# Performance work log

Hardware: AMD Instinct MI355X
Metric: run time of the kernel (lower is better)

## Reference

```python
import jax, jax.numpy as jnp
import numpy as np

HIDDEN = 1280
NUM_HEADS = 16
HEAD_DIM = HIDDEN // NUM_HEADS  # 80
ROPE_DIM = HEAD_DIM // 2        # 40
THETA = 10000.0
SEQ = 3072


def setup_inputs() -> dict:
    key = jax.random.key(0)
    ks = jax.random.split(key, 6)
    hidden_states = jax.random.normal(ks[0], (SEQ, HIDDEN), dtype=jnp.float32)
    position_ids = jax.random.randint(ks[1], (SEQ, 2), 0, 64, dtype=jnp.int32)
    qkv_w = jax.random.normal(ks[2], (HIDDEN, 3 * HIDDEN), dtype=jnp.float32) * (HIDDEN ** -0.5)
    qkv_b = jax.random.normal(ks[3], (3 * HIDDEN,), dtype=jnp.float32) * 0.02
    o_w = jax.random.normal(ks[4], (HIDDEN, HIDDEN), dtype=jnp.float32) * (HIDDEN ** -0.5)
    o_b = jax.random.normal(ks[5], (HIDDEN,), dtype=jnp.float32) * 0.02
    return {"hidden_states": hidden_states, "position_ids": position_ids,
            "qkv_w": qkv_w, "qkv_b": qkv_b, "o_w": o_w, "o_b": o_b}


def _rotate_half(x):
    x1, x2 = jnp.split(x, 2, axis=-1)
    return jnp.concatenate([-x2, x1], axis=-1)


def reference(hidden_states, position_ids, qkv_w, qkv_b, o_w, o_b):
    seq_len = hidden_states.shape[0]
    # fused QKV projection
    qkv = hidden_states @ qkv_w + qkv_b                     # (S, 3*H*D)
    qkv = qkv.reshape(seq_len, 3, NUM_HEADS, HEAD_DIM)
    q, k, v = qkv[:, 0], qkv[:, 1], qkv[:, 2]               # each (S, h, d)
    # 2D RoPE: inv_freq over rope dim = head_dim // 2
    inv_freq = 1.0 / (THETA ** (jnp.arange(0, ROPE_DIM, 2, dtype=jnp.float32) / ROPE_DIM))
    pos = position_ids.astype(jnp.float32)
    h_freqs = jnp.outer(pos[:, 0], inv_freq)                # (S, rope/2)
    w_freqs = jnp.outer(pos[:, 1], inv_freq)                # (S, rope/2)
    freqs = jnp.concatenate([h_freqs, w_freqs], axis=-1)    # (S, rope)
    emb = jnp.concatenate([freqs, freqs], axis=-1)          # (S, head_dim)
    cos = jnp.cos(emb)[:, None, :]                          # (S, 1, d)
    sin = jnp.sin(emb)[:, None, :]
    q = q * cos + _rotate_half(q) * sin
    k = k * cos + _rotate_half(k) * sin
    # manual attention
    scaling = HEAD_DIM ** -0.5
    attn = jnp.einsum('qhd,khd->hqk', q * scaling, k)       # (h, S, S)
    attn = jax.nn.softmax(attn, axis=-1)
    out = jnp.einsum('hqk,khd->qhd', attn, v)               # (S, h, d)
    out = out.reshape(seq_len, HIDDEN)
    return out @ o_w + o_b
```

## Files before the change

### kernel.cpp

```cpp
#include <hip/hip_runtime.h>

#define SEQ  3072
#define HID  1280
#define NH   16
#define HD   80
#define NQKV 3840

typedef unsigned short u16;
typedef unsigned int u32;
typedef __attribute__((ext_vector_type(8))) short short8;
typedef __attribute__((ext_vector_type(4))) float floatx4;

__device__ __forceinline__ u16 f2bf(float x) {
    u32 u = __float_as_uint(x);
    u += 0x7fffu + ((u >> 16) & 1u);
    return (u16)(u >> 16);
}
__device__ __forceinline__ u32 packrne(float a, float b) {
    return (u32)f2bf(a) | ((u32)f2bf(b) << 16);
}

typedef const __attribute__((address_space(1))) unsigned int* gp1_t;
typedef __attribute__((address_space(3))) unsigned int* lp3_t;
__device__ __forceinline__ void gld16(const void* g, void* l) {
    __builtin_amdgcn_global_load_lds((gp1_t)g, (lp3_t)l, 16, 0, 0);
}

__device__ __forceinline__ int swz_qk(int c, int r) {
    return (c < 8) ? (c ^ (r & 7)) : (8 + ((c - 8) ^ ((r >> 1) & 3)));
}

__global__ void rope_tables_k(const int* __restrict__ pos, float* __restrict__ cosb,
                              float* __restrict__ sinb) {
    int s = blockIdx.x;
    int j = threadIdx.x;
    if (j >= 40) return;
    float p = (float)((j < 20) ? pos[s * 2] : pos[s * 2 + 1]);
    int i = (j < 20) ? j : j - 20;
    float inv = powf(10000.0f, -(float)i / 20.0f);
    float a = p * inv;
    cosb[s * 40 + j] = cosf(a);
    sinb[s * 40 + j] = sinf(a);
}

__global__ void cast_bf16_k(const float* __restrict__ x, u16* __restrict__ hi, int n) {
    int i = blockIdx.x * 256 + threadIdx.x;
    if (i >= n) return;
    hi[i] = f2bf(x[i]);
}

__global__ void transpose_cast_k(const float* __restrict__ w, u16* __restrict__ thi,
                                 int K, int N) {
    __shared__ float tile[32][33];
    int n0 = blockIdx.x * 32, k0 = blockIdx.y * 32;
    int c = threadIdx.x & 31, r8 = threadIdx.x >> 5;
    for (int rr = r8; rr < 32; rr += 8)
        tile[rr][c] = w[(size_t)(k0 + rr) * N + n0 + c];
    __syncthreads();
    for (int rr = r8; rr < 32; rr += 8)
        thi[(size_t)(n0 + rr) * K + k0 + c] = f2bf(tile[c][rr]);
}

__global__ __launch_bounds__(256, 3) void gemm_bf16_k(
    const u16* __restrict__ A, const u16* __restrict__ B,
    const float* __restrict__ bias, float* __restrict__ C,
    int M, int N, int K) {
    __shared__ u16 lA[128 * 64], lB[128 * 64];
    const int t = threadIdx.x, lane = t & 63, w = t >> 6;
    const int qi = lane & 15, quad = lane >> 4;
    const int m0 = blockIdx.y * 128, n0 = blockIdx.x * 128;
    const int wm = (w >> 1) * 64, wn = (w & 1) * 64;

    floatx4 acc[4][4];
    for (int mi = 0; mi < 4; mi++)
        for (int ni = 0; ni < 4; ni++) acc[mi][ni] = (floatx4){0.f, 0.f, 0.f, 0.f};

    const int rg = lane >> 3;
    const int ce = ((lane & 7) ^ rg) * 8;
    size_t gA[4], gB[4];
    for (int g = 0; g < 4; g++) {
        int row = w * 32 + g * 8 + rg;
        gA[g] = (size_t)(m0 + row) * K + ce;
        gB[g] = (size_t)(n0 + row) * K + ce;
    }

    for (int k0 = 0; k0 < K; k0 += 64) {
        for (int g = 0; g < 4; g++) {
            gld16(A + gA[g] + k0, &lA[(w * 32 + g * 8) * 64]);
            gld16(B + gB[g] + k0, &lB[(w * 32 + g * 8) * 64]);
        }
        __syncthreads();
        short8 af[4][2], bf[4][2];
        for (int mi = 0; mi < 4; mi++) {
            int row = wm + mi * 16 + qi;
            for (int kh = 0; kh < 2; kh++)
                af[mi][kh] = *(const short8*)&lA[row * 64 + (((kh * 4 + quad) ^ (row & 7)) << 3)];
        }
        for (int ni = 0; ni < 4; ni++) {
            int row = wn + ni * 16 + qi;
            for (int kh = 0; kh < 2; kh++)
                bf[ni][kh] = *(const short8*)&lB[row * 64 + (((kh * 4 + quad) ^ (row & 7)) << 3)];
        }
        for (int mi = 0; mi < 4; mi++)
            for (int ni = 0; ni < 4; ni++) {
                acc[mi][ni] = __builtin_amdgcn_mfma_f32_16x16x32_bf16(af[mi][0], bf[ni][0], acc[mi][ni], 0, 0, 0);
                acc[mi][ni] = __builtin_amdgcn_mfma_f32_16x16x32_bf16(af[mi][1], bf[ni][1], acc[mi][ni], 0, 0, 0);
            }
        __syncthreads();
    }
    for (int mi = 0; mi < 4; mi++)
        for (int ni = 0; ni < 4; ni++) {
            int col = n0 + wn + ni * 16 + qi;
            int rowb = m0 + wm + mi * 16 + quad * 4;
            float b = bias[col];
            for (int r = 0; r < 4; r++)
                C[(size_t)(rowb + r) * N + col] = acc[mi][ni][r] + b;
        }
}

__global__ void pack_qkv_k(const float* __restrict__ qkv, const float* __restrict__ cosb,
                           const float* __restrict__ sinb,
                           u16* __restrict__ Qs, u16* __restrict__ Ks, u16* __restrict__ Vs) {
    __shared__ float lv[80 * 65];
    const int t = threadIdx.x;
    const int h = blockIdx.y, s0 = blockIdx.x * 64;
    const float qsc = 0.11180339887498949f * 1.4426950408889634f;

    for (int i = t; i < 64 * 10; i += 256) {
        int rl = i / 10, jg = i % 10;
        int s = s0 + rl, j = jg * 4;
        const float4 cc = *(const float4*)&cosb[s * 40 + j];
        const float4 ss = *(const float4*)&sinb[s * 40 + j];
        const float* qb = qkv + (size_t)s * NQKV + h * HD;
        const float4 q1 = *(const float4*)&qb[j];
        const float4 q2 = *(const float4*)&qb[j + 40];
        const float* kb = qb + HID;
        const float4 k1 = *(const float4*)&kb[j];
        const float4 k2 = *(const float4*)&kb[j + 40];
        uint2 qo1, qo2, ko1, ko2;
        qo1.x = packrne((q1.x * cc.x - q2.x * ss.x) * qsc, (q1.y * cc.y - q2.y * ss.y) * qsc);
        qo1.y = packrne((q1.z * cc.z - q2.z * ss.z) * qsc, (q1.w * cc.w - q2.w * ss.w) * qsc);
        qo2.x = packrne((q2.x * cc.x + q1.x * ss.x) * qsc, (q2.y * cc.y + q1.y * ss.y) * qsc);
        qo2.y = packrne((q2.z * cc.z + q1.z * ss.z) * qsc, (q2.w * cc.w + q1.w * ss.w) * qsc);
        ko1.x = packrne(k1.x * cc.x - k2.x * ss.x, k1.y * cc.y - k2.y * ss.y);
        ko1.y = packrne(k1.z * cc.z - k2.z * ss.z, k1.w * cc.w - k2.w * ss.w);
        ko2.x = packrne(k2.x * cc.x + k1.x * ss.x, k2.y * cc.y + k1.y * ss.y);
        ko2.y = packrne(k2.z * cc.z + k1.z * ss.z, k2.w * cc.w + k1.w * ss.w);
        size_t base = (size_t)(h * SEQ + s) * 96;
        int c0 = j >> 3, sub0 = j & 7;
        int c1 = (j + 40) >> 3, sub1 = (j + 40) & 7;
        int p0 = swz_qk(c0, s);
        int p1 = swz_qk(c1, s);
        *(uint2*)&Qs[base + p0 * 8 + sub0] = qo1;
        *(uint2*)&Qs[base + p1 * 8 + sub1] = qo2;
        *(uint2*)&Ks[base + p0 * 8 + sub0] = ko1;
        *(uint2*)&Ks[base + p1 * 8 + sub1] = ko2;
    }
    for (int i = t; i < 64 * 2; i += 256) {
        int rl = i >> 1, cz = 10 + (i & 1);
        int s = s0 + rl;
        int pz = swz_qk(cz, s);
        size_t base = (size_t)(h * SEQ + s) * 96;
        *(uint4*)&Qs[base + pz * 8] = (uint4){0, 0, 0, 0};
        *(uint4*)&Ks[base + pz * 8] = (uint4){0, 0, 0, 0};
    }
    for (int i = t; i < 64 * 80; i += 256) {
        int rl = i / 80, d = i % 80;
        lv[d * 65 + rl] = qkv[(size_t)(s0 + rl) * NQKV + 2 * HID + h * HD + d];
    }
    __syncthreads();
    for (int i = t; i < 80 * 16; i += 256) {
        int d = i / 16, g = i % 16;
        int c2l = g * 4;
        float v0 = lv[d * 65 + c2l], v1 = lv[d * 65 + c2l + 1];
        float v2 = lv[d * 65 + c2l + 2], v3 = lv[d * 65 + c2l + 3];
        int pc = (g >> 1) ^ (d & 7);
        uint2 o;
        o.x = packrne(v0, v1);
        o.y = packrne(v2, v3);
        *(uint2*)&Vs[((size_t)h * HD + d) * SEQ + s0 + pc * 8 + (g & 1) * 4] = o;
    }
}

__global__ __launch_bounds__(256, 3) void attn_k(
    const u16* __restrict__ Qs, const u16* __restrict__ Ks, const u16* __restrict__ Vs,
    float* __restrict__ Op, float* __restrict__ lp) {
    __shared__ u16 kbuf[2][6144];
    __shared__ u16 vbuf[2][5120];
    __shared__ u16 pls[4][1024];

    const int t = threadIdx.x, lane = t & 63, w = t >> 6;
    const int qi = lane & 15, quad = lane >> 4;
    const int h = blockIdx.y, q0 = blockIdx.x * 128, ksp = blockIdx.z;
    const int kc0 = ksp * (SEQ / 2);
    u16* const kflat = &kbuf[0][0];

    {
        const u16* Qt = Qs + (size_t)(h * SEQ + q0) * 96;
        for (int j = 0; j < 6; j++) {
            int o = (w * 6 + j) * 512;
            gld16(Qt + o + lane * 8, kflat + o);
        }
    }
    __syncthreads();
    short8 bq[2][3];
    for (int qg = 0; qg < 2; qg++) {
        int row = w * 32 + qg * 16 + qi;
        for (int k3 = 0; k3 < 3; k3++) {
            int p = (k3 < 2) ? ((4 * k3 + quad) ^ (qi & 7)) : (8 + (quad ^ ((qi >> 1) & 3)));
            bq[qg][k3] = *(const short8*)&kflat[(row * 12 + p) * 8];
        }
    }
    __syncthreads();

    float l_lane[2] = {0.f, 0.f};
    floatx4 acco[2][5];
    for (int qg = 0; qg < 2; qg++)
        for (int dt = 0; dt < 5; dt++) acco[qg][dt] = (floatx4){0.f, 0.f, 0.f, 0.f};

    auto stage = [&](int it, int buf) {
        int kc = kc0 + it * 64;
        const u16* Kt = Ks + (size_t)(h * SEQ + kc) * 96;
        for (int j = 0; j < 3; j++) {
            int o = (w * 3 + j) * 512;
            gld16(Kt + o + lane * 8, &kbuf[buf][o]);
        }
        const u16* Vt = Vs + (size_t)h * HD * SEQ + kc;
        for (int i = w; i < 10; i += 4) {
            int p16 = i * 64 + lane;
            int d = p16 >> 3, pc = p16 & 7;
            gld16(Vt + (size_t)d * SEQ + pc * 8, &vbuf[buf][i * 512]);
        }
    };
    stage(0, 0);
    __syncthreads();

    const int NT = (SEQ / 2) / 64;
    char* const myp = (char*)&pls[w][0];
    for (int it = 0; it < NT; it++) {
        int cur = it & 1;
        if (it + 1 < NT) stage(it + 1, cur ^ 1);
        const u16* kb = &kbuf[cur][0];
        const u16* vb = &vbuf[cur][0];
        for (int c2 = 0; c2 < 2; c2++) {
            for (int ktl = 0; ktl < 2; ktl++) {
                int kt = c2 * 2 + ktl;
                int arow = kt * 16 + qi;
                short8 ak[3];
                for (int k3 = 0; k3 < 3; k3++) {
                    int p = (k3 < 2) ? ((4 * k3 + quad) ^ (qi & 7)) : (8 + (quad ^ ((qi >> 1) & 3)));
                    ak[k3] = *(const short8*)&kb[(arow * 12 + p) * 8];
                }
                for (int qg = 0; qg < 2; qg++) {
                    floatx4 s = (floatx4){0.f, 0.f, 0.f, 0.f};
                    s = __builtin_amdgcn_mfma_f32_16x16x32_bf16(ak[0], bq[qg][0], s, 0, 0, 0);
                    s = __builtin_amdgcn_mfma_f32_16x16x32_bf16(ak[1], bq[qg][1], s, 0, 0, 0);
                    s = __builtin_amdgcn_mfma_f32_16x16x32_bf16(ak[2], bq[qg][2], s, 0, 0, 0);
                    float e0 = __builtin_amdgcn_exp2f(s[0]);
                    float e1 = __builtin_amdgcn_exp2f(s[1]);
                    float e2 = __builtin_amdgcn_exp2f(s[2]);
                    float e3 = __builtin_amdgcn_exp2f(s[3]);
                    l_lane[qg] += (e0 + e1) + (e2 + e3);
                    uint2 pk;
                    pk.x = __builtin_amdgcn_perm(__float_as_uint(e1), __float_as_uint(e0), 0x07060302u);
                    pk.y = __builtin_amdgcn_perm(__float_as_uint(e3), __float_as_uint(e2), 0x07060302u);
                    int chunk = qg * 4 + 2 * ktl + (quad >> 1);
                    *(uint2*)(myp + qi * 128 + ((chunk ^ (qi & 7)) << 4) + ((quad & 1) << 3)) = pk;
                }
            }
            short8 bp0 = *(const short8*)(myp + qi * 128 + (((quad) ^ (qi & 7)) << 4));
            short8 bp1 = *(const short8*)(myp + qi * 128 + (((4 + quad) ^ (qi & 7)) << 4));
            int pv = (4 * c2 + quad) ^ (qi & 7);
            for (int dt = 0; dt < 5; dt++) {
                short8 av = *(const short8*)&vb[((dt * 16 + qi) * 8 + pv) * 8];
                acco[0][dt] = __builtin_amdgcn_mfma_f32_16x16x32_bf16(av, bp0, acco[0][dt], 0, 0, 0);
                acco[1][dt] = __builtin_amdgcn_mfma_f32_16x16x32_bf16(av, bp1, acco[1][dt], 0, 0, 0);
            }
        }
        __syncthreads();
    }

    for (int qg = 0; qg < 2; qg++) {
        float lq = l_lane[qg];
        lq += __shfl_xor(lq, 16);
        lq += __shfl_xor(lq, 32);
        int q = q0 + w * 32 + qg * 16 + qi;
        if (quad == 0) lp[(size_t)(ksp * NH + h) * SEQ + q] = lq;
        for (int dt = 0; dt < 5; dt++)
            for (int r = 0; r < 4; r++) {
                int d = dt * 16 + quad * 4 + r;
                Op[((size_t)(ksp * NH + h) * HD + d) * SEQ + q] = acco[qg][dt][r];
            }
    }
}

__global__ void merge_k(const float* __restrict__ Op, const float* __restrict__ lp,
                        u16* __restrict__ att) {
    __shared__ float ls[HD * 65];
    __shared__ float li[64];
    const int t = threadIdx.x;
    const int h = blockIdx.y, q0 = blockIdx.x * 64;
    for (int i = t; i < HD * 16; i += 256) {
        int d = i / 16, g = i % 16;
        size_t a0 = ((size_t)h * HD + d) * SEQ + q0 + g * 4;
        size_t a1 = ((size_t)(NH + h) * HD + d) * SEQ + q0 + g * 4;
        const float4 v0 = *(const float4*)&Op[a0];
        const float4 v1 = *(const float4*)&Op[a1];
        ls[d * 65 + g * 4 + 0] = v0.x + v1.x;
        ls[d * 65 + g * 4 + 1] = v0.y + v1.y;
        ls[d * 65 + g * 4 + 2] = v0.z + v1.z;
        ls[d * 65 + g * 4 + 3] = v0.w + v1.w;
    }
    if (t < 64)
        li[t] = 1.0f / (lp[(size_t)h * SEQ + q0 + t] + lp[(size_t)(NH + h) * SEQ + q0 + t]);
    __syncthreads();
    for (int i = t; i < 64 * 40; i += 256) {
        int ql = i / 40, dg = i % 40;
        int d0 = dg * 2;
        float s = li[ql];
        u32 o = packrne(ls[d0 * 65 + ql] * s, ls[(d0 + 1) * 65 + ql] * s);
        *(u32*)&att[(size_t)(q0 + ql) * HID + h * HD + d0] = o;
    }
}

extern "C" void kernel_launch(void* const* d_in, const int* in_sizes, int n_in,
                              void* d_out, int out_size, void* d_ws, size_t ws_size,
                              hipStream_t stream) {
    const float* hs   = (const float*)d_in[0];
    const int*   pos  = (const int*)d_in[1];
    const float* qkvw = (const float*)d_in[2];
    const float* qkvb = (const float*)d_in[3];
    const float* ow   = (const float*)d_in[4];
    const float* ob   = (const float*)d_in[5];
    float* out = (float*)d_out;

    char* p = (char*)d_ws;
    auto alloc = [&](size_t bytes) {
        char* r = p;
        p += (bytes + 255) & ~(size_t)255;
        return r;
    };
    float* cosb = (float*)alloc((size_t)SEQ * 40 * 4);
    float* sinb = (float*)alloc((size_t)SEQ * 40 * 4);
    u16* owT = (u16*)alloc((size_t)HID * HID * 2);
    char* pool1 = alloc(18874368 + 9437184);
    u16* hH = (u16*)pool1;
    u16* wT = (u16*)(pool1 + 7864320);
    u16* Qs = (u16*)pool1;
    u16* Ks = (u16*)(pool1 + 9437184);
    char* pool2 = alloc((size_t)SEQ * NQKV * 4);
    float* qkv_s = (float*)pool2;
    u16* att  = (u16*)pool2;
    float* Op = (float*)(pool2 + 7864320);
    float* lp = (float*)(pool2 + 39321600);
    u16* Vs = (u16*)alloc((size_t)NH * HD * SEQ * 2);

    hipLaunchKernelGGL(rope_tables_k, dim3(SEQ), dim3(64), 0, stream, pos, cosb, sinb);
    hipLaunchKernelGGL(cast_bf16_k, dim3((SEQ * HID + 255) / 256), dim3(256), 0, stream,
                       hs, hH, SEQ * HID);
    hipLaunchKernelGGL(transpose_cast_k, dim3(NQKV / 32, HID / 32), dim3(256), 0, stream,
                       qkvw, wT, HID, NQKV);
    hipLaunchKernelGGL(transpose_cast_k, dim3(HID / 32, HID / 32), dim3(256), 0, stream,
                       ow, owT, HID, HID);
    hipLaunchKernelGGL(gemm_bf16_k, dim3(NQKV / 128, SEQ / 128), dim3(256), 0, stream,
                       hH, wT, qkvb, qkv_s, SEQ, NQKV, HID);
    hipLaunchKernelGGL(pack_qkv_k, dim3(SEQ / 64, NH), dim3(256), 0, stream,
                       qkv_s, cosb, sinb, Qs, Ks, Vs);
    hipLaunchKernelGGL(attn_k, dim3(SEQ / 128, NH, 2), dim3(256), 0, stream,
                       Qs, Ks, Vs, Op, lp);
    hipLaunchKernelGGL(merge_k, dim3(SEQ / 64, NH), dim3(256), 0, stream, Op, lp, att);
    hipLaunchKernelGGL(gemm_bf16_k, dim3(HID / 128, SEQ / 128), dim3(256), 0, stream,
                       att, owT, ob, out, SEQ, HID, HID);
}
```

Baseline: 248.8 us.

## Restructure attention to 192-query tiles, 3-way key split, unpadded head dim, fused prep

Merges the four preprocessing kernels into one launch. The QKV and output GEMMs get an XCD-aware block-to-tile mapping. Q/K are stored unpadded at 80 columns, and the third MFMA k-step takes a half-width load padded with zeros. Attention now uses 192-query tiles with three query groups per wave and splits keys three ways for better CU occupancy, and Op is written row-major so the merge becomes a simple vectorized elementwise kernel. The intent is to cut launch overhead, memory traffic and L2 misses, at the cost of more registers and an extra partial-output buffer.

```diff
diff --git a/kernel.cpp b/kernel.cpp
--- a/kernel.cpp
+++ b/kernel.cpp
@@ -5,10 +5,15 @@
 #define NH   16
 #define HD   80
 #define NQKV 3840
+#define KSP  3
+#define QT   192
+#define KCHUNK 1024
+#define NT   16
 
 typedef unsigned short u16;
 typedef unsigned int u32;
 typedef __attribute__((ext_vector_type(8))) short short8;
+typedef __attribute__((ext_vector_type(4))) short short4v;
 typedef __attribute__((ext_vector_type(4))) float floatx4;
 
 __device__ __forceinline__ u16 f2bf(float x) {
@@ -26,49 +31,72 @@
     __builtin_amdgcn_global_load_lds((gp1_t)g, (lp3_t)l, 16, 0, 0);
 }
 
-__device__ __forceinline__ int swz_qk(int c, int r) {
-    return (c < 8) ? (c ^ (r & 7)) : (8 + ((c - 8) ^ ((r >> 1) & 3)));
-}
-
-__global__ void rope_tables_k(const int* __restrict__ pos, float* __restrict__ cosb,
-                              float* __restrict__ sinb) {
-    int s = blockIdx.x;
-    int j = threadIdx.x;
-    if (j >= 40) return;
-    float p = (float)((j < 20) ? pos[s * 2] : pos[s * 2 + 1]);
-    int i = (j < 20) ? j : j - 20;
-    float inv = powf(10000.0f, -(float)i / 20.0f);
-    float a = p * inv;
-    cosb[s * 40 + j] = cosf(a);
-    sinb[s * 40 + j] = sinf(a);
-}
-
-__global__ void cast_bf16_k(const float* __restrict__ x, u16* __restrict__ hi, int n) {
-    int i = blockIdx.x * 256 + threadIdx.x;
-    if (i >= n) return;
-    hi[i] = f2bf(x[i]);
-}
-
-__global__ void transpose_cast_k(const float* __restrict__ w, u16* __restrict__ thi,
-                                 int K, int N) {
+__device__ __forceinline__ int swz80(int c, int r) {
+    return (c < 8) ? (c ^ (r & 7)) : (8 + ((c - 8) ^ ((r >> 2) & 1)));
+}
+
+__global__ void prep_k(const int* __restrict__ pos, float* __restrict__ cosb,
+                       float* __restrict__ sinb, const float* __restrict__ hs,
+                       u16* __restrict__ hH, const float* __restrict__ qkvw,
+                       u16* __restrict__ wT, const float* __restrict__ ow,
+                       u16* __restrict__ owT) {
     __shared__ float tile[32][33];
-    int n0 = blockIdx.x * 32, k0 = blockIdx.y * 32;
-    int c = threadIdx.x & 31, r8 = threadIdx.x >> 5;
-    for (int rr = r8; rr < 32; rr += 8)
-        tile[rr][c] = w[(size_t)(k0 + rr) * N + n0 + c];
-    __syncthreads();
-    for (int rr = r8; rr < 32; rr += 8)
-        thi[(size_t)(n0 + rr) * K + k0 + c] = f2bf(tile[c][rr]);
+    const int b = blockIdx.x, t = threadIdx.x;
+    if (b < 480) {
+        int i = b * 256 + t;
+        int s = i / 40, j = i % 40;
+        float p = (float)((j < 20) ? pos[s * 2] : pos[s * 2 + 1]);
+        int k = (j < 20) ? j : j - 20;
+        float inv = powf(10000.0f, -(float)k / 20.0f);
+        float a = p * inv;
+        cosb[s * 40 + j] = cosf(a);
+        sinb[s * 40 + j] = sinf(a);
+    } else if (b < 4320) {
+        int i = (b - 480) * 256 + t;
+        const float4 x = ((const float4*)hs)[i];
+        uint2 o;
+        o.x = packrne(x.x, x.y);
+        o.y = packrne(x.z, x.w);
+        ((uint2*)hH)[i] = o;
+    } else {
+        const float* w;
+        u16* dst;
+        int K, N, nx, ky;
+        if (b < 9120) {
+            int i = b - 4320;
+            nx = i % 120; ky = i / 120; w = qkvw; dst = wT; K = HID; N = NQKV;
+        } else {
+            int i = b - 9120;
+            nx = i % 40; ky = i / 40; w = ow; dst = owT; K = HID; N = HID;
+        }
+        int n0 = nx * 32, k0 = ky * 32;
+        int c = t & 31, r8 = t >> 5;
+        for (int rr = r8; rr < 32; rr += 8)
+            tile[rr][c] = w[(size_t)(k0 + rr) * N + n0 + c];
+        __syncthreads();
+        for (int rr = r8; rr < 32; rr += 8)
+            dst[(size_t)(n0 + rr) * K + k0 + c] = f2bf(tile[c][rr]);
+    }
 }
 
 __global__ __launch_bounds__(256, 3) void gemm_bf16_k(
     const u16* __restrict__ A, const u16* __restrict__ B,
     const float* __restrict__ bias, float* __restrict__ C,
-    int M, int N, int K) {
+    int M, int N, int K, int mode) {
     __shared__ u16 lA[128 * 64], lB[128 * 64];
     const int t = threadIdx.x, lane = t & 63, w = t >> 6;
     const int qi = lane & 15, quad = lane >> 4;
-    const int m0 = blockIdx.y * 128, n0 = blockIdx.x * 128;
+    int id = blockIdx.x;
+    int xcd = id & 7, sN = id >> 3;
+    int m_idx, n_idx;
+    if (mode == 0) {
+        n_idx = (xcd & 1) * 15 + sN % 15;
+        m_idx = (xcd >> 1) * 6 + sN / 15;
+    } else {
+        m_idx = xcd * 3 + sN / 10;
+        n_idx = sN % 10;
+    }
+    const int m0 = m_idx * 128, n0 = n_idx * 128;
     const int wm = (w >> 1) * 64, wn = (w & 1) * 64;
 
     floatx4 acc[4][4];
@@ -146,23 +174,14 @@
         ko1.y = packrne(k1.z * cc.z - k2.z * ss.z, k1.w * cc.w - k2.w * ss.w);
         ko2.x = packrne(k2.x * cc.x + k1.x * ss.x, k2.y * cc.y + k1.y * ss.y);
         ko2.y = packrne(k2.z * cc.z + k1.z * ss.z, k2.w * cc.w + k1.w * ss.w);
-        size_t base = (size_t)(h * SEQ + s) * 96;
-        int c0 = j >> 3, sub0 = j & 7;
-        int c1 = (j + 40) >> 3, sub1 = (j + 40) & 7;
-        int p0 = swz_qk(c0, s);
-        int p1 = swz_qk(c1, s);
+        size_t base = (size_t)(h * SEQ + s) * 80;
+        int sub0 = j & 7, sub1 = (j + 40) & 7;
+        int p0 = swz80(j >> 3, s);
+        int p1 = swz80((j + 40) >> 3, s);
         *(uint2*)&Qs[base + p0 * 8 + sub0] = qo1;
         *(uint2*)&Qs[base + p1 * 8 + sub1] = qo2;
         *(uint2*)&Ks[base + p0 * 8 + sub0] = ko1;
         *(uint2*)&Ks[base + p1 * 8 + sub1] = ko2;
-    }
-    for (int i = t; i < 64 * 2; i += 256) {
-        int rl = i >> 1, cz = 10 + (i & 1);
-        int s = s0 + rl;
-        int pz = swz_qk(cz, s);
-        size_t base = (size_t)(h * SEQ + s) * 96;
-        *(uint4*)&Qs[base + pz * 8] = (uint4){0, 0, 0, 0};
-        *(uint4*)&Ks[base + pz * 8] = (uint4){0, 0, 0, 0};
     }
     for (int i = t; i < 64 * 80; i += 256) {
         int rl = i / 80, d = i % 80;
@@ -185,46 +204,58 @@
 __global__ __launch_bounds__(256, 3) void attn_k(
     const u16* __restrict__ Qs, const u16* __restrict__ Ks, const u16* __restrict__ Vs,
     float* __restrict__ Op, float* __restrict__ lp) {
-    __shared__ u16 kbuf[2][6144];
+    __shared__ u16 kbuf[2][5120];
     __shared__ u16 vbuf[2][5120];
     __shared__ u16 pls[4][1024];
 
     const int t = threadIdx.x, lane = t & 63, w = t >> 6;
     const int qi = lane & 15, quad = lane >> 4;
-    const int h = blockIdx.y, q0 = blockIdx.x * 128, ksp = blockIdx.z;
-    const int kc0 = ksp * (SEQ / 2);
+    const int id = blockIdx.x;
+    const int xcd = id & 7, sI = id >> 3;
+    const int c = xcd * 6 + (sI >> 4);
+    const int h = c & 15, ksp = c >> 4;
+    const int q0 = (sI & 15) * QT;
+    const int kc0 = ksp * KCHUNK;
     u16* const kflat = &kbuf[0][0];
 
-    {
-        const u16* Qt = Qs + (size_t)(h * SEQ + q0) * 96;
-        for (int j = 0; j < 6; j++) {
-            int o = (w * 6 + j) * 512;
-            gld16(Qt + o + lane * 8, kflat + o);
-        }
-    }
-    __syncthreads();
-    short8 bq[2][3];
-    for (int qg = 0; qg < 2; qg++) {
-        int row = w * 32 + qg * 16 + qi;
-        for (int k3 = 0; k3 < 3; k3++) {
-            int p = (k3 < 2) ? ((4 * k3 + quad) ^ (qi & 7)) : (8 + (quad ^ ((qi >> 1) & 3)));
-            bq[qg][k3] = *(const short8*)&kflat[(row * 12 + p) * 8];
-        }
-    }
-    __syncthreads();
-
-    float l_lane[2] = {0.f, 0.f};
-    floatx4 acco[2][5];
-    for (int qg = 0; qg < 2; qg++)
+    const u16* Qt = Qs + (size_t)(h * SEQ + q0) * 80;
+    for (int j = 0; j < 5; j++) {
+        int o = (w * 5 + j) * 512;
+        gld16(Qt + o + lane * 8, kflat + o);
+    }
+    __syncthreads();
+    short8 bq[3][3];
+    auto qfrag = [&](const u16* basep, int rowl, int qg) {
+        const u16* rb = &basep[rowl * 80];
+        bq[qg][0] = *(const short8*)&rb[(quad ^ (qi & 7)) << 3];
+        bq[qg][1] = *(const short8*)&rb[((4 + quad) ^ (qi & 7)) << 3];
+        short4v t2 = *(const short4v*)&rb[((8 + ((quad >> 1) ^ ((qi >> 2) & 1))) << 3) + ((quad & 1) << 2)];
+        bq[qg][2] = (short8){t2.x, t2.y, t2.z, t2.w, 0, 0, 0, 0};
+    };
+    for (int qg = 0; qg < 3; qg++) {
+        int row0 = w * 48 + qg * 16;
+        if (row0 < 128) qfrag(kflat, row0 + qi, qg);
+    }
+    __syncthreads();
+    for (int i = w; i < 10; i += 4)
+        gld16(Qt + 128 * 80 + i * 512 + lane * 8, &kbuf[0][i * 512]);
+    __syncthreads();
+    for (int qg = 0; qg < 3; qg++) {
+        int row0 = w * 48 + qg * 16;
+        if (row0 >= 128) qfrag(&kbuf[0][0], row0 - 128 + qi, qg);
+    }
+    __syncthreads();
+
+    float l_lane[3] = {0.f, 0.f, 0.f};
+    floatx4 acco[3][5];
+    for (int qg = 0; qg < 3; qg++)
         for (int dt = 0; dt < 5; dt++) acco[qg][dt] = (floatx4){0.f, 0.f, 0.f, 0.f};
 
-    auto stage = [&](int it, int buf) {
-        int kc = kc0 + it * 64;
-        const u16* Kt = Ks + (size_t)(h * SEQ + kc) * 96;
-        for (int j = 0; j < 3; j++) {
-            int o = (w * 3 + j) * 512;
-            gld16(Kt + o + lane * 8, &kbuf[buf][o]);
-        }
+    auto stage = [&](int it2, int buf) {
+        int kc = kc0 + it2 * 64;
+        const u16* Kt = Ks + (size_t)(h * SEQ + kc) * 80;
+        for (int i = w; i < 10; i += 4)
+            gld16(Kt + i * 512 + lane * 8, &kbuf[buf][i * 512]);
         const u16* Vt = Vs + (size_t)h * HD * SEQ + kc;
         for (int i = w; i < 10; i += 4) {
             int p16 = i * 64 + lane;
@@ -235,7 +266,6 @@
     stage(0, 0);
     __syncthreads();
 
-    const int NT = (SEQ / 2) / 64;
     char* const myp = (char*)&pls[w][0];
     for (int it = 0; it < NT; it++) {
         int cur = it & 1;
@@ -243,19 +273,25 @@
         const u16* kb = &kbuf[cur][0];
         const u16* vb = &vbuf[cur][0];
         for (int c2 = 0; c2 < 2; c2++) {
+            short8 av[5];
+            {
+                int pvc = (4 * c2 + quad) ^ (qi & 7);
+                for (int dt = 0; dt < 5; dt++)
+                    av[dt] = *(const short8*)&vb[((dt * 16 + qi) * 8 + pvc) * 8];
+            }
+            uint2 pk2[2];
             for (int ktl = 0; ktl < 2; ktl++) {
-                int kt = c2 * 2 + ktl;
-                int arow = kt * 16 + qi;
-                short8 ak[3];
-                for (int k3 = 0; k3 < 3; k3++) {
-                    int p = (k3 < 2) ? ((4 * k3 + quad) ^ (qi & 7)) : (8 + (quad ^ ((qi >> 1) & 3)));
-                    ak[k3] = *(const short8*)&kb[(arow * 12 + p) * 8];
-                }
-                for (int qg = 0; qg < 2; qg++) {
+                int arow = (c2 * 2 + ktl) * 16 + qi;
+                const u16* rb = &kb[arow * 80];
+                short8 a0 = *(const short8*)&rb[(quad ^ (qi & 7)) << 3];
+                short8 a1 = *(const short8*)&rb[((4 + quad) ^ (qi & 7)) << 3];
+                short4v a2v = *(const short4v*)&rb[((8 + ((quad >> 1) ^ ((qi >> 2) & 1))) << 3) + ((quad & 1) << 2)];
+                short8 a2 = (short8){a2v.x, a2v.y, a2v.z, a2v.w, 0, 0, 0, 0};
+                for (int qg = 0; qg < 3; qg++) {
                     floatx4 s = (floatx4){0.f, 0.f, 0.f, 0.f};
-                    s = __builtin_amdgcn_mfma_f32_16x16x32_bf16(ak[0], bq[qg][0], s, 0, 0, 0);
-                    s = __builtin_amdgcn_mfma_f32_16x16x32_bf16(ak[1], bq[qg][1], s, 0, 0, 0);
-                    s = __builtin_amdgcn_mfma_f32_16x16x32_bf16(ak[2], bq[qg][2], s, 0, 0, 0);
+                    s = __builtin_amdgcn_mfma_f32_16x16x32_bf16(a0, bq[qg][0], s, 0, 0, 0);
+                    s = __builtin_amdgcn_mfma_f32_16x16x32_bf16(a1, bq[qg][1], s, 0, 0, 0);
+                    s = __builtin_amdgcn_mfma_f32_16x16x32_bf16(a2, bq[qg][2], s, 0, 0, 0);
                     float e0 = __builtin_amdgcn_exp2f(s[0]);
                     float e1 = __builtin_amdgcn_exp2f(s[1]);
                     float e2 = __builtin_amdgcn_exp2f(s[2]);
@@ -264,63 +300,60 @@
                     uint2 pk;
                     pk.x = __builtin_amdgcn_perm(__float_as_uint(e1), __float_as_uint(e0), 0x07060302u);
                     pk.y = __builtin_amdgcn_perm(__float_as_uint(e3), __float_as_uint(e2), 0x07060302u);
-                    int chunk = qg * 4 + 2 * ktl + (quad >> 1);
-                    *(uint2*)(myp + qi * 128 + ((chunk ^ (qi & 7)) << 4) + ((quad & 1) << 3)) = pk;
+                    if (qg < 2) {
+                        int chunk = qg * 4 + 2 * ktl + (quad >> 1);
+                        *(uint2*)(myp + qi * 128 + ((chunk ^ (qi & 7)) << 4) + ((quad & 1) << 3)) = pk;
+                    } else {
+                        pk2[ktl] = pk;
+                    }
                 }
             }
-            short8 bp0 = *(const short8*)(myp + qi * 128 + (((quad) ^ (qi & 7)) << 4));
+            short8 bp0 = *(const short8*)(myp + qi * 128 + ((quad ^ (qi & 7)) << 4));
             short8 bp1 = *(const short8*)(myp + qi * 128 + (((4 + quad) ^ (qi & 7)) << 4));
-            int pv = (4 * c2 + quad) ^ (qi & 7);
             for (int dt = 0; dt < 5; dt++) {
-                short8 av = *(const short8*)&vb[((dt * 16 + qi) * 8 + pv) * 8];
-                acco[0][dt] = __builtin_amdgcn_mfma_f32_16x16x32_bf16(av, bp0, acco[0][dt], 0, 0, 0);
-                acco[1][dt] = __builtin_amdgcn_mfma_f32_16x16x32_bf16(av, bp1, acco[1][dt], 0, 0, 0);
+                acco[0][dt] = __builtin_amdgcn_mfma_f32_16x16x32_bf16(av[dt], bp0, acco[0][dt], 0, 0, 0);
+                acco[1][dt] = __builtin_amdgcn_mfma_f32_16x16x32_bf16(av[dt], bp1, acco[1][dt], 0, 0, 0);
             }
+            for (int ktl = 0; ktl < 2; ktl++) {
+                int chunk = 2 * ktl + (quad >> 1);
+                *(uint2*)(myp + qi * 128 + ((chunk ^ (qi & 7)) << 4) + ((quad & 1) << 3)) = pk2[ktl];
+            }
+            short8 bp2 = *(const short8*)(myp + qi * 128 + ((quad ^ (qi & 7)) << 4));
+            for (int dt = 0; dt < 5; dt++)
+                acco[2][dt] = __builtin_amdgcn_mfma_f32_16x16x32_bf16(av[dt], bp2, acco[2][dt], 0, 0, 0);
         }
         __syncthreads();
     }
 
-    for (int qg = 0; qg < 2; qg++) {
+    for (int qg = 0; qg < 3; qg++) {
         float lq = l_lane[qg];
         lq += __shfl_xor(lq, 16);
         lq += __shfl_xor(lq, 32);
-        int q = q0 + w * 32 + qg * 16 + qi;
-        if (quad == 0) lp[(size_t)(ksp * NH + h) * SEQ + q] = lq;
+        int q = q0 + w * 48 + qg * 16 + qi;
+        if (quad == 0) lp[((size_t)ksp * NH + h) * SEQ + q] = lq;
+        float* ob = &Op[(((size_t)ksp * NH + h) * SEQ + q) * HD];
         for (int dt = 0; dt < 5; dt++)
-            for (int r = 0; r < 4; r++) {
-                int d = dt * 16 + quad * 4 + r;
-                Op[((size_t)(ksp * NH + h) * HD + d) * SEQ + q] = acco[qg][dt][r];
-            }
+            *(floatx4*)&ob[dt * 16 + quad * 4] = acco[qg][dt];
     }
 }
 
 __global__ void merge_k(const float* __restrict__ Op, const float* __restrict__ lp,
                         u16* __restrict__ att) {
-    __shared__ float ls[HD * 65];
-    __shared__ float li[64];
-    const int t = threadIdx.x;
-    const int h = blockIdx.y, q0 = blockIdx.x * 64;
-    for (int i = t; i < HD * 16; i += 256) {
-        int d = i / 16, g = i % 16;
-        size_t a0 = ((size_t)h * HD + d) * SEQ + q0 + g * 4;
-        size_t a1 = ((size_t)(NH + h) * HD + d) * SEQ + q0 + g * 4;
-        const float4 v0 = *(const float4*)&Op[a0];
-        const float4 v1 = *(const float4*)&Op[a1];
-        ls[d * 65 + g * 4 + 0] = v0.x + v1.x;
-        ls[d * 65 + g * 4 + 1] = v0.y + v1.y;
-        ls[d * 65 + g * 4 + 2] = v0.z + v1.z;
-        ls[d * 65 + g * 4 + 3] = v0.w + v1.w;
-    }
-    if (t < 64)
-        li[t] = 1.0f / (lp[(size_t)h * SEQ + q0 + t] + lp[(size_t)(NH + h) * SEQ + q0 + t]);
-    __syncthreads();
-    for (int i = t; i < 64 * 40; i += 256) {
-        int ql = i / 40, dg = i % 40;
-        int d0 = dg * 2;
-        float s = li[ql];
-        u32 o = packrne(ls[d0 * 65 + ql] * s, ls[(d0 + 1) * 65 + ql] * s);
-        *(u32*)&att[(size_t)(q0 + ql) * HID + h * HD + d0] = o;
-    }
+    int g = blockIdx.x * 256 + threadIdx.x;
+    int h = g / (SEQ * 20);
+    int r = g % (SEQ * 20);
+    int q = r / 20, dg = r % 20;
+    float sx = 0.f, sy = 0.f, sz = 0.f, sw = 0.f, l = 0.f;
+    for (int ksp = 0; ksp < KSP; ksp++) {
+        const float4 v = *(const float4*)&Op[(((size_t)ksp * NH + h) * SEQ + q) * HD + dg * 4];
+        sx += v.x; sy += v.y; sz += v.z; sw += v.w;
+        l += lp[((size_t)ksp * NH + h) * SEQ + q];
+    }
+    float li = 1.0f / l;
+    uint2 o;
+    o.x = packrne(sx * li, sy * li);
+    o.y = packrne(sz * li, sw * li);
+    *(uint2*)&att[(size_t)q * HID + h * HD + dg * 4] = o;
 }
 
 extern "C" void kernel_launch(void* const* d_in, const int* in_sizes, int n_in,
@@ -343,32 +376,27 @@
     float* cosb = (float*)alloc((size_t)SEQ * 40 * 4);
     float* sinb = (float*)alloc((size_t)SEQ * 40 * 4);
     u16* owT = (u16*)alloc((size_t)HID * HID * 2);
-    char* pool1 = alloc(18874368 + 9437184);
+    char* pool1 = alloc(7864320 + 9830400);
     u16* hH = (u16*)pool1;
     u16* wT = (u16*)(pool1 + 7864320);
     u16* Qs = (u16*)pool1;
-    u16* Ks = (u16*)(pool1 + 9437184);
-    char* pool2 = alloc((size_t)SEQ * NQKV * 4);
+    u16* Ks = (u16*)(pool1 + 7864320);
+    char* pool2 = alloc(55640320);
     float* qkv_s = (float*)pool2;
     u16* att  = (u16*)pool2;
     float* Op = (float*)(pool2 + 7864320);
-    float* lp = (float*)(pool2 + 39321600);
+    float* lp = (float*)(pool2 + 7864320 + 47185920);
     u16* Vs = (u16*)alloc((size_t)NH * HD * SEQ * 2);
 
-    hipLaunchKernelGGL(rope_tables_k, dim3(SEQ), dim3(64), 0, stream, pos, cosb, sinb);
-    hipLaunchKernelGGL(cast_bf16_k, dim3((SEQ * HID + 255) / 256), dim3(256), 0, stream,
-                       hs, hH, SEQ * HID);
-    hipLaunchKernelGGL(transpose_cast_k, dim3(NQKV / 32, HID / 32), dim3(256), 0, stream,
-                       qkvw, wT, HID, NQKV);
-    hipLaunchKernelGGL(transpose_cast_k, dim3(HID / 32, HID / 32), dim3(256), 0, stream,
-                       ow, owT, HID, HID);
-    hipLaunchKernelGGL(gemm_bf16_k, dim3(NQKV / 128, SEQ / 128), dim3(256), 0, stream,
-                       hH, wT, qkvb, qkv_s, SEQ, NQKV, HID);
+    hipLaunchKernelGGL(prep_k, dim3(10720), dim3(256), 0, stream,
+                       pos, cosb, sinb, hs, hH, qkvw, wT, ow, owT);
+    hipLaunchKernelGGL(gemm_bf16_k, dim3(720), dim3(256), 0, stream,
+                       hH, wT, qkvb, qkv_s, SEQ, NQKV, HID, 0);
     hipLaunchKernelGGL(pack_qkv_k, dim3(SEQ / 64, NH), dim3(256), 0, stream,
                        qkv_s, cosb, sinb, Qs, Ks, Vs);
-    hipLaunchKernelGGL(attn_k, dim3(SEQ / 128, NH, 2), dim3(256), 0, stream,
+    hipLaunchKernelGGL(attn_k, dim3(768), dim3(256), 0, stream,
                        Qs, Ks, Vs, Op, lp);
-    hipLaunchKernelGGL(merge_k, dim3(SEQ / 64, NH), dim3(256), 0, stream, Op, lp, att);
-    hipLaunchKernelGGL(gemm_bf16_k, dim3(HID / 128, SEQ / 128), dim3(256), 0, stream,
-                       att, owT, ob, out, SEQ, HID, HID);
-}
+    hipLaunchKernelGGL(merge_k, dim3(3840), dim3(256), 0, stream, Op, lp, att);
+    hipLaunchKernelGGL(gemm_bf16_k, dim3(240), dim3(256), 0, stream,
+                       att, owT, ob, out, SEQ, HID, HID, 1);
+}
```

Result: slower. 392.4 us (+57.7%).
